# Kernel tuning notes

Measured on AMD Instinct MI355X. Metric: run time of the kernel, lower is better.

The kernel has to match this reference:

```python
import jax, jax.numpy as jnp
import numpy as np

Q_HEADS, KV_HEADS, HEAD_DIM, WINDOW = 16, 4, 128, 512
HIDDEN = 2048
ROPE_BASE = 10000.0


def _rope_tables(T, head_dim, dtype):
    half = head_dim // 2
    inv_freq = 1.0 / (ROPE_BASE ** (jnp.arange(half, dtype=jnp.float32) / half))
    t = jnp.arange(T, dtype=jnp.float32)
    freqs = jnp.outer(t, inv_freq)  # [T, half]
    return jnp.cos(freqs).astype(dtype), jnp.sin(freqs).astype(dtype)


def _apply_rope(x, cos, sin):
    # x: [B, T, H, D]; cos/sin: [T, D//2] -> broadcast [1, T, 1, D//2]
    c = cos[None, :, None, :]
    s = sin[None, :, None, :]
    x1, x2 = jnp.split(x, 2, axis=-1)
    return jnp.concatenate([x1 * c - x2 * s, x1 * s + x2 * c], axis=-1)


def setup_inputs() -> dict:
    key = jax.random.key(0)
    ks = jax.random.split(key, 5)
    B, T = 1, 4096
    x = jax.random.normal(ks[0], (B, T, HIDDEN), dtype=jnp.float32)
    sc = 0.02
    wq = jax.random.normal(ks[1], (Q_HEADS * HEAD_DIM, HIDDEN), dtype=jnp.float32) * sc
    wk = jax.random.normal(ks[2], (KV_HEADS * HEAD_DIM, HIDDEN), dtype=jnp.float32) * sc
    wv = jax.random.normal(ks[3], (KV_HEADS * HEAD_DIM, HIDDEN), dtype=jnp.float32) * sc
    wo = jax.random.normal(ks[4], (HIDDEN, Q_HEADS * HEAD_DIM), dtype=jnp.float32) * sc
    return {"x": x, "wq": wq, "wk": wk, "wv": wv, "wo": wo}


def reference(x, wq, wk, wv, wo):
    B, T, _ = x.shape
    reps = Q_HEADS // KV_HEADS
    scale = 1.0 / np.sqrt(HEAD_DIM)

    q = jnp.einsum('bth,oh->bto', x, wq).reshape(B, T, Q_HEADS, HEAD_DIM)
    k = jnp.einsum('bth,oh->bto', x, wk).reshape(B, T, KV_HEADS, HEAD_DIM)
    v = jnp.einsum('bth,oh->bto', x, wv).reshape(B, T, KV_HEADS, HEAD_DIM)

    cos, sin = _rope_tables(T, HEAD_DIM, x.dtype)
    q = _apply_rope(q, cos, sin)
    k = _apply_rope(k, cos, sin)

    # GQA without materializing repeated K/V: group q as [B,T,KVH,reps,D]
    qg = q.reshape(B, T, KV_HEADS, reps, HEAD_DIM)
    scores = jnp.einsum('btgrd,bsgd->bgrts', qg, k) * scale  # [B,KVH,reps,T,T]

    idx = jnp.arange(T)
    # allowed: causal (s <= t) AND within window (t - s <= WINDOW)
    allowed = (idx[None, :] <= idx[:, None]) & (idx[:, None] - idx[None, :] <= WINDOW)
    scores = jnp.where(allowed[None, None, None], scores, jnp.finfo(scores.dtype).min)
    probs = jax.nn.softmax(scores, axis=-1)

    out = jnp.einsum('bgrts,bsgd->btgrd', probs, v)  # [B,T,KVH,reps,D]
    out = out.reshape(B, T, Q_HEADS * HEAD_DIM)
    return jnp.einsum('bto,ho->bth', out, wo)
```

## Files before the change

### kernel.cpp

```cpp
#include <hip/hip_runtime.h>

typedef __attribute__((ext_vector_type(8))) short short8;
typedef __attribute__((ext_vector_type(4))) float f32x4;
typedef __attribute__((ext_vector_type(4))) unsigned short u16x4;

__device__ __forceinline__ unsigned short f2b(float f) {
  unsigned int u = __float_as_uint(f);
  u += 0x7fffu + ((u >> 16) & 1u);
  return (unsigned short)(u >> 16);
}
__device__ __forceinline__ void glds16(const void* g, void* l) {
  __builtin_amdgcn_global_load_lds(
      (const __attribute__((address_space(1))) unsigned int*)g,
      (__attribute__((address_space(3))) unsigned int*)l, 16, 0, 0);
}

__global__ __launch_bounds__(256) void cast_all(const float* __restrict__ x,
                                                const float* __restrict__ wq,
                                                const float* __restrict__ wk,
                                                const float* __restrict__ wv,
                                                const float* __restrict__ wo,
                                                unsigned short* __restrict__ dst) {
  const int i = blockIdx.x * 256 + threadIdx.x;
  const float* s;
  int off;
  if (i < 2097152)      { s = x;  off = i; }
  else if (i < 3145728) { s = wq; off = i - 2097152; }
  else if (i < 3407872) { s = wk; off = i - 3145728; }
  else if (i < 3670016) { s = wv; off = i - 3407872; }
  else                  { s = wo; off = i - 3670016; }
  f32x4 v = ((const f32x4*)s)[off];
  u16x4 o;
  o[0] = f2b(v[0]); o[1] = f2b(v[1]); o[2] = f2b(v[2]); o[3] = f2b(v[3]);
  ((u16x4*)dst)[i] = o;
}

__global__ __launch_bounds__(512, 2) void gemm256(
    const unsigned short* __restrict__ A, const unsigned short* __restrict__ B,
    const int Karg, const int mode,
    unsigned short* __restrict__ qb, unsigned short* __restrict__ kb,
    unsigned short* __restrict__ vtg, float* __restrict__ Cout, const int Narg) {
  extern __shared__ char smem[];
  const int tid = threadIdx.x;
  const int w = tid >> 6, lane = tid & 63;
  const int quad = lane >> 4, l15 = lane & 15;
  const int wm = w >> 2, wn = w & 3;
  const int m0 = blockIdx.x * 256, n0 = blockIdx.y * 256;

  int nb[4];
#pragma unroll
  for (int ni = 0; ni < 4; ++ni) {
    const int bbi = (wn & 1) * 4 + ni;
    nb[ni] = mode ? ((bbi & 1) ? 4 + (bbi >> 1) : (bbi >> 1)) : bbi;
  }

  const int fragOff = l15 * 64 + ((quad * 16) ^ ((l15 & 8) << 2));
  char* const aWave = smem + wm * 16384;
  char* const bWave = smem + 32768 + (wn >> 1) * 16384;

  const int sr = lane >> 2;
  const int sc = ((lane & 3) * 8) ^ ((lane & 32) ? 16 : 0);
  const unsigned short* const Abase = A + (size_t)(m0 + (w >> 1) * 16 + sr) * 2048 + (w & 1) * 32 + sc;
  const unsigned short* const Bbase = B + (size_t)(n0 + (w >> 1) * 16 + sr) * 2048 + (w & 1) * 32 + sc;

#define BARF()                            \
  asm volatile("" ::: "memory");          \
  __builtin_amdgcn_s_barrier();           \
  asm volatile("" ::: "memory");

#define STAGE_AJ(h, tt, jj)                                                              \
  {                                                                                      \
    const int t_ = ((tt) < 32) ? (tt) : 31;                                              \
    glds16(Abase + (size_t)(h) * (128 * 2048) + (jj) * (64 * 2048) + (size_t)t_ * 64,    \
           smem + (t_ & 1) * 65536 + (h) * 16384 + (jj) * 8192 + w * 1024);              \
  }
#define STAGE_B2(h, tt)                                                                  \
  {                                                                                      \
    const int t_ = ((tt) < 32) ? (tt) : 31;                                              \
    char* const d_ = smem + (t_ & 1) * 65536 + 32768 + (h) * 16384 + w * 1024;           \
    glds16(Bbase + (size_t)(h) * (128 * 2048) + (size_t)t_ * 64, d_);                    \
    glds16(Bbase + (size_t)(h) * (128 * 2048) + (64 * 2048) + (size_t)t_ * 64, d_ + 8192); \
  }
#define RD_A(dst, c, MI0)                                                                \
  _Pragma("unroll") for (int mi = 0; mi < 4; ++mi)                                       \
  _Pragma("unroll") for (int kk = 0; kk < 2; ++kk)                                       \
      dst[mi][kk] = *(const short8*)(aWave + (c) * 65536 + (((MI0) + mi) * 2 + kk) * 1024 + fragOff);
#define RD_B(dst, c, NI0)                                                                \
  _Pragma("unroll") for (int ni = 0; ni < 2; ++ni)                                       \
  _Pragma("unroll") for (int kk = 0; kk < 2; ++kk)                                       \
      dst[ni][kk] = *(const short8*)(bWave + (c) * 65536 + (nb[(NI0) + ni] * 2 + kk) * 1024 + fragOff);

  f32x4 acc[8][4];
  const f32x4 fz = {0.f, 0.f, 0.f, 0.f};
#pragma unroll
  for (int i = 0; i < 8; ++i)
#pragma unroll
    for (int j = 0; j < 4; ++j) acc[i][j] = fz;

  short8 af[4][2], blo[2][2], bhi[2][2];

#define MFMA_Q(MOFF, NOFF, BF)                                                   \
  _Pragma("unroll") for (int mi = 0; mi < 4; ++mi)                               \
  _Pragma("unroll") for (int ni = 0; ni < 2; ++ni)                               \
  _Pragma("unroll") for (int kk = 0; kk < 2; ++kk)                               \
      acc[(MOFF) + mi][(NOFF) + ni] = __builtin_amdgcn_mfma_f32_16x16x32_bf16(   \
          af[mi][kk], BF[ni][kk], acc[(MOFF) + mi][(NOFF) + ni], 0, 0, 0);

  STAGE_AJ(0, 0, 0) STAGE_AJ(1, 0, 0) STAGE_B2(0, 0) STAGE_B2(1, 0) STAGE_AJ(0, 0, 1) STAGE_AJ(1, 0, 1)
  STAGE_AJ(0, 1, 0) STAGE_AJ(1, 1, 0) STAGE_B2(0, 1) STAGE_B2(1, 1) STAGE_AJ(0, 1, 1) STAGE_AJ(1, 1, 1)
  asm volatile("s_waitcnt vmcnt(8)" ::: "memory");
  __builtin_amdgcn_s_barrier();
  asm volatile("" ::: "memory");
  RD_A(af, 0, 0)
  RD_B(blo, 0, 0)

#define HALF(c, tt)                                                                  \
                                                                             \
  BARF()                                                                             \
  __builtin_amdgcn_s_setprio(1); MFMA_Q(0, 0, blo) __builtin_amdgcn_s_setprio(0);    \
  RD_B(bhi, (c), 2)                                                                  \
  BARF()                                                                             \
   STAGE_AJ(0, (tt) + 2, 0) STAGE_AJ(1, (tt) + 2, 0)                         \
  BARF()                                                                             \
  __builtin_amdgcn_s_setprio(1); MFMA_Q(0, 2, bhi) __builtin_amdgcn_s_setprio(0);    \
  RD_A(af, (c), 4)                                                                   \
  BARF()                                                                             \
   STAGE_B2(0, (tt) + 2) STAGE_B2(1, (tt) + 2)                               \
  BARF()                                                                             \
  __builtin_amdgcn_s_setprio(1); MFMA_Q(4, 2, bhi) __builtin_amdgcn_s_setprio(0);    \
  BARF()                                                                             \
   STAGE_AJ(0, (tt) + 2, 1) STAGE_AJ(1, (tt) + 2, 1)                         \
  BARF()                                                                             \
  __builtin_amdgcn_s_setprio(1); MFMA_Q(4, 0, blo) __builtin_amdgcn_s_setprio(0);    \
  asm volatile("s_waitcnt vmcnt(8)" ::: "memory");                                   \
  RD_A(af, (c) ^ 1, 0)                                                               \
  RD_B(blo, (c) ^ 1, 0)

#pragma unroll 1
  for (int T = 0; T < 32; T += 2) {
    HALF(0, T)
    HALF(1, T + 1)
  }
  asm volatile("s_waitcnt vmcnt(0)" ::: "memory");
#undef HALF
#undef MFMA_Q
#undef RD_A
#undef RD_B
#undef STAGE_AJ
#undef STAGE_B2
#undef BARF

  if (mode == 0) {
    const int colBase = n0 + wn * 64;
#pragma unroll
    for (int mi = 0; mi < 8; ++mi) {
      const int row = m0 + wm * 128 + mi * 16 + quad * 4;
#pragma unroll
      for (int ni = 0; ni < 4; ++ni) {
        const int col = colBase + ni * 16 + l15;
#pragma unroll
        for (int r = 0; r < 4; ++r)
          Cout[(size_t)(row + r) * 2048 + col] = acc[mi][ni][r];
      }
    }
    return;
  }

  const int y = blockIdx.y;
  const int tb0 = m0 + wm * 128;
  if (y >= 10) {
    const int g = (y - 10) * 2 + (wn >> 1);
#pragma unroll
    for (int mi = 0; mi < 8; ++mi) {
      const int tb = tb0 + mi * 16 + quad * 4;
#pragma unroll
      for (int ni = 0; ni < 4; ++ni) {
        const int d = nb[ni] * 16 + l15;
        u16x4 o;
#pragma unroll
        for (int r = 0; r < 4; ++r) o[r] = f2b(acc[mi][ni][r]);
        *(u16x4*)(vtg + (size_t)(g * 128 + d) * 4096 + tb) = o;
      }
    }
  } else {
    unsigned short* dst;
    int stride, hoff;
    if (y < 8) { dst = qb; stride = 2048; hoff = (y * 2 + (wn >> 1)) * 128; }
    else       { dst = kb; stride = 512;  hoff = ((y - 8) * 2 + (wn >> 1)) * 128; }
    const float c2 = 0.20762050593045889f;
    const float inv2pi = 0.15915494309189535f;
#pragma unroll
    for (int j = 0; j < 2; ++j) {
      const int i = ((wn & 1) * 2 + j) * 16 + l15;
      const float inv_rev = exp2f(-(float)i * c2) * inv2pi;
#pragma unroll
      for (int mi = 0; mi < 8; ++mi) {
#pragma unroll
        for (int r = 0; r < 4; ++r) {
          const int t = tb0 + mi * 16 + quad * 4 + r;
          float rev = (float)t * inv_rev;
          rev -= floorf(rev);
          const float sn = __builtin_amdgcn_sinf(rev);
          const float cs = __builtin_amdgcn_cosf(rev);
          const float x1 = acc[mi][2 * j][r], x2 = acc[mi][2 * j + 1][r];
          unsigned short* p = dst + (size_t)t * stride + hoff + i;
          p[0]  = f2b(x1 * cs - x2 * sn);
          p[64] = f2b(x1 * sn + x2 * cs);
        }
      }
    }
  }
}

__global__ __launch_bounds__(512) void attn_fwd(const unsigned short* __restrict__ qp,
                                                const unsigned short* __restrict__ kp,
                                                const unsigned short* __restrict__ vtg,
                                                unsigned short* __restrict__ op) {
  __shared__ unsigned short Ks[2][4][1024];
  __shared__ unsigned short Vt[2][4096];
  const int tid = threadIdx.x;
  const int w = tid >> 6, lane = tid & 63;
  const int quad = lane >> 4, l15 = lane & 15;
  const int t0 = blockIdx.x * 64;
  const int g = blockIdx.y;
  const int h = g * 4 + (w & 3);
  const int t0w = t0 + (w >> 2) * 32;
  const f32x4 fzero = {0.f, 0.f, 0.f, 0.f};
  const float scale = 0.088388347648318447f;
  const float NEG_INF = -__builtin_inff();

  short8 qf[4][2];
#pragma unroll
  for (int qt = 0; qt < 2; qt++) {
    const unsigned short* qrow = qp + (size_t)(t0w + qt * 16 + l15) * 2048 + h * 128 + quad * 8;
#pragma unroll
    for (int kb = 0; kb < 4; kb++) qf[kb][qt] = *(const short8*)(qrow + kb * 32);
  }

  f32x4 oacc[8][2];
#pragma unroll
  for (int db = 0; db < 8; db++) { oacc[db][0] = fzero; oacc[db][1] = fzero; }
  float Mrow[2] = {-1.0e30f, -1.0e30f}, Lrow[2] = {0.f, 0.f};

  const int s_begin = (t0 >= 512) ? (t0 - 512) : 0;
  const int nch = ((t0 + 63 - s_begin) >> 5) + 1;

  const int r4 = lane >> 2, c4 = lane & 3;
#define ATTN_STAGE(s0_, b_)                                                              \
  {                                                                                      \
    const int s0v = (s0_);                                                               \
    if (w < 4) {                                                                         \
      _Pragma("unroll")                                                                  \
      for (int p = 0; p < 2; p++)                                                        \
        glds16(kp + (size_t)(s0v + p * 16 + r4) * 512 + g * 128 + w * 32 + c4 * 8,       \
               &Ks[b_][w][p * 512]);                                                     \
    } else {                                                                             \
      const int wv = w - 4;                                                              \
      _Pragma("unroll")                                                                  \
      for (int p = 0; p < 2; p++)                                                        \
        glds16(vtg + (size_t)(g * 128 + wv * 32 + p * 16 + r4) * 4096 + s0v + c4 * 8,    \
               &Vt[b_][wv * 1024 + p * 512]);                                            \
    }                                                                                    \
  }

  ATTN_STAGE(s_begin, 0);

  for (int c = 0; c < nch; ++c) {
    const int s0 = s_begin + c * 32;
    const int b = c & 1;
    __syncthreads();
    if (c + 1 < nch) ATTN_STAGE(s_begin + (c + 1) * 32, (c + 1) & 1);

    if (s0 + 31 >= t0w - 512 && s0 <= t0w + 31) {
      f32x4 sacc[2][2];
      sacc[0][0] = fzero; sacc[0][1] = fzero; sacc[1][0] = fzero; sacc[1][1] = fzero;
      const int permBase = ((l15 >> 2) << 3) + (l15 & 3);
#pragma unroll
      for (int kb = 0; kb < 4; kb++) {
        short8 af0 = *(const short8*)&Ks[b][kb][(permBase + 0) * 32 + quad * 8];
        short8 af1 = *(const short8*)&Ks[b][kb][(permBase + 4) * 32 + quad * 8];
        sacc[0][0] = __builtin_amdgcn_mfma_f32_16x16x32_bf16(af0, qf[kb][0], sacc[0][0], 0, 0, 0);
        sacc[0][1] = __builtin_amdgcn_mfma_f32_16x16x32_bf16(af0, qf[kb][1], sacc[0][1], 0, 0, 0);
        sacc[1][0] = __builtin_amdgcn_mfma_f32_16x16x32_bf16(af1, qf[kb][0], sacc[1][0], 0, 0, 0);
        sacc[1][1] = __builtin_amdgcn_mfma_f32_16x16x32_bf16(af1, qf[kb][1], sacc[1][1], 0, 0, 0);
      }

      short8 pb[2];
      float alpha[2];
#pragma unroll
      for (int qt = 0; qt < 2; qt++) {
        const int tq = t0w + qt * 16 + l15;
        float vals[8];
        float cmax = NEG_INF;
#pragma unroll
        for (int kt = 0; kt < 2; kt++)
#pragma unroll
          for (int r = 0; r < 4; r++) {
            const int s = s0 + quad * 8 + kt * 4 + r;
            const bool ok = (unsigned)(tq - s) <= 512u;
            const float v = ok ? sacc[kt][qt][r] * scale : NEG_INF;
            vals[kt * 4 + r] = v;
            cmax = fmaxf(cmax, v);
          }
        cmax = fmaxf(cmax, __shfl_xor(cmax, 16));
        cmax = fmaxf(cmax, __shfl_xor(cmax, 32));
        const float Mnew = fmaxf(Mrow[qt], cmax);
        alpha[qt] = __expf(Mrow[qt] - Mnew);
        Mrow[qt] = Mnew;
        float csum = 0.f;
#pragma unroll
        for (int j = 0; j < 8; j++) {
          const float p = __expf(vals[j] - Mnew);
          csum += p;
          pb[qt][j] = (short)f2b(p);
        }
        csum += __shfl_xor(csum, 16);
        csum += __shfl_xor(csum, 32);
        Lrow[qt] = Lrow[qt] * alpha[qt] + csum;
      }

#pragma unroll
      for (int db = 0; db < 8; db++) {
        short8 vf = *(const short8*)&Vt[b][(db * 16 + l15) * 32 + quad * 8];
#pragma unroll
        for (int qt = 0; qt < 2; qt++) {
          oacc[db][qt][0] *= alpha[qt]; oacc[db][qt][1] *= alpha[qt];
          oacc[db][qt][2] *= alpha[qt]; oacc[db][qt][3] *= alpha[qt];
          oacc[db][qt] = __builtin_amdgcn_mfma_f32_16x16x32_bf16(vf, pb[qt], oacc[db][qt], 0, 0, 0);
        }
      }
    }
  }
#undef ATTN_STAGE

#pragma unroll
  for (int qt = 0; qt < 2; qt++) {
    const float invL = 1.f / Lrow[qt];
    unsigned short* orow = op + (size_t)(t0w + qt * 16 + l15) * 2048 + h * 128;
#pragma unroll
    for (int db = 0; db < 8; db++) {
      u16x4 o;
#pragma unroll
      for (int r = 0; r < 4; r++) o[r] = f2b(oacc[db][qt][r] * invL);
      *(u16x4*)(orow + db * 16 + quad * 4) = o;
    }
  }
}

extern "C" void kernel_launch(void* const* d_in, const int* in_sizes, int n_in,
                              void* d_out, int out_size, void* d_ws, size_t ws_size,
                              hipStream_t stream) {
  const float* x  = (const float*)d_in[0];
  const float* wq = (const float*)d_in[1];
  const float* wk = (const float*)d_in[2];
  const float* wv = (const float*)d_in[3];
  const float* wo = (const float*)d_in[4];
  float* out = (float*)d_out;
  char* ws = (char*)d_ws;

  unsigned short* xb    = (unsigned short*)(ws + 0);
  unsigned short* wqkv  = (unsigned short*)(ws + 16777216);
  unsigned short* wob   = (unsigned short*)(ws + 29360128);
  unsigned short* qb    = (unsigned short*)(ws + 37748736);
  unsigned short* kbuf  = (unsigned short*)(ws + 54525952);
  unsigned short* vtg   = (unsigned short*)(ws + 58720256);
  unsigned short* attnb = xb;

  static bool attr_done = false;
  if (!attr_done) {
    hipFuncSetAttribute(reinterpret_cast<const void*>(gemm256),
                        hipFuncAttributeMaxDynamicSharedMemorySize, 131072);
    attr_done = true;
  }

  cast_all<<<18432, 256, 0, stream>>>(x, wq, wk, wv, wo, (unsigned short*)ws);

  gemm256<<<dim3(16, 12), 512, 131072, stream>>>(xb, wqkv, 2048, 1,
                                                 qb, kbuf, vtg, nullptr, 0);

  attn_fwd<<<dim3(64, 4), 512, 0, stream>>>(qb, kbuf, vtg, attnb);

  gemm256<<<dim3(16, 8), 512, 131072, stream>>>(attnb, wob, 2048, 0,
                                                nullptr, nullptr, nullptr, out, 2048);
}
```

Measured before the change: 261.8 us.

## Add 128x256-tile output-projection GEMM kernel for more blocks

```diff
diff --git a/kernel.cpp b/kernel.cpp
--- a/kernel.cpp
+++ b/kernel.cpp
@@ -212,6 +212,118 @@
   }
 }
 
+__global__ __launch_bounds__(512, 2) void gemm128(const unsigned short* __restrict__ A,
+                                                  const unsigned short* __restrict__ B,
+                                                  float* __restrict__ Cout) {
+  extern __shared__ char smem[];
+  const int tid = threadIdx.x;
+  const int w = tid >> 6, lane = tid & 63;
+  const int quad = lane >> 4, l15 = lane & 15;
+  const int wm = w >> 2, wn = w & 3;
+  const int m0 = blockIdx.x * 128, n0 = blockIdx.y * 256;
+
+  const int fragOff = l15 * 64 + ((quad * 16) ^ ((l15 & 8) << 2));
+  char* const aWave = smem;
+  char* const bWave = smem + 16384 + (wn >> 1) * 16384;
+
+  const int sr = lane >> 2;
+  const int sc = ((lane & 3) * 8) ^ ((lane & 32) ? 16 : 0);
+  const unsigned short* const Abase = A + (size_t)(m0 + (w >> 1) * 16 + sr) * 2048 + (w & 1) * 32 + sc;
+  const unsigned short* const Bbase = B + (size_t)(n0 + (w >> 1) * 16 + sr) * 2048 + (w & 1) * 32 + sc;
+
+#define BARF()                            \
+  asm volatile("" ::: "memory");          \
+  __builtin_amdgcn_s_barrier();           \
+  asm volatile("" ::: "memory");
+
+#define G_STAGE_A(tt)                                                                    \
+  {                                                                                      \
+    const int t_ = ((tt) < 32) ? (tt) : 31;                                              \
+    char* const d_ = smem + (t_ & 1) * 49152 + w * 1024;                                 \
+    glds16(Abase + (size_t)t_ * 64, d_);                                                 \
+    glds16(Abase + (64 * 2048) + (size_t)t_ * 64, d_ + 8192);                            \
+  }
+#define G_STAGE_B(h, tt)                                                                 \
+  {                                                                                      \
+    const int t_ = ((tt) < 32) ? (tt) : 31;                                              \
+    char* const d_ = smem + (t_ & 1) * 49152 + 16384 + (h) * 16384 + w * 1024;           \
+    glds16(Bbase + (size_t)(h) * (128 * 2048) + (size_t)t_ * 64, d_);                    \
+    glds16(Bbase + (size_t)(h) * (128 * 2048) + (64 * 2048) + (size_t)t_ * 64, d_ + 8192); \
+  }
+#define G_RD_A(c)                                                                        \
+  _Pragma("unroll") for (int mi = 0; mi < 4; ++mi)                                       \
+  _Pragma("unroll") for (int kk = 0; kk < 2; ++kk)                                       \
+      af[mi][kk] = *(const short8*)(aWave + (c) * 49152 + ((wm * 4 + mi) * 2 + kk) * 1024 + fragOff);
+#define G_RD_B(dst, c, NI0)                                                              \
+  _Pragma("unroll") for (int ni = 0; ni < 2; ++ni)                                       \
+  _Pragma("unroll") for (int kk = 0; kk < 2; ++kk)                                       \
+      dst[ni][kk] = *(const short8*)(bWave + (c) * 49152 + (((wn & 1) * 4 + (NI0) + ni) * 2 + kk) * 1024 + fragOff);
+
+  f32x4 acc[4][4];
+  const f32x4 fz = {0.f, 0.f, 0.f, 0.f};
+#pragma unroll
+  for (int i = 0; i < 4; ++i)
+#pragma unroll
+    for (int j = 0; j < 4; ++j) acc[i][j] = fz;
+
+  short8 af[4][2], blo[2][2], bhi[2][2];
+
+#define G_MFMA(NOFF, BF)                                                         \
+  _Pragma("unroll") for (int mi = 0; mi < 4; ++mi)                               \
+  _Pragma("unroll") for (int ni = 0; ni < 2; ++ni)                               \
+  _Pragma("unroll") for (int kk = 0; kk < 2; ++kk)                               \
+      acc[mi][(NOFF) + ni] = __builtin_amdgcn_mfma_f32_16x16x32_bf16(            \
+          af[mi][kk], BF[ni][kk], acc[mi][(NOFF) + ni], 0, 0, 0);
+
+  G_STAGE_A(0) G_STAGE_B(0, 0) G_STAGE_B(1, 0) G_STAGE_A(1)
+  asm volatile("s_waitcnt vmcnt(2)" ::: "memory");
+  __builtin_amdgcn_s_barrier();
+  asm volatile("" ::: "memory");
+  G_RD_A(0)
+  G_RD_B(blo, 0, 0)
+
+#define G_TILE(c, tt)                                                                \
+   G_STAGE_B(0, (tt) + 1) G_STAGE_B(1, (tt) + 1)                             \
+  BARF()                                                                             \
+  __builtin_amdgcn_s_setprio(1); G_MFMA(0, blo) __builtin_amdgcn_s_setprio(0);       \
+  G_RD_B(bhi, (c), 2)                                                                \
+  BARF()                                                                             \
+   G_STAGE_A((tt) + 2)                                                       \
+  BARF()                                                                             \
+  __builtin_amdgcn_s_setprio(1); G_MFMA(2, bhi) __builtin_amdgcn_s_setprio(0);       \
+  asm volatile("s_waitcnt vmcnt(2)" ::: "memory");                                   \
+  G_RD_A((c) ^ 1)                                                                    \
+  G_RD_B(blo, (c) ^ 1, 0)                                                            \
+  BARF()
+
+#pragma unroll 1
+  for (int T = 0; T < 32; T += 2) {
+    G_TILE(0, T)
+    G_TILE(1, T + 1)
+  }
+  asm volatile("s_waitcnt vmcnt(0)" ::: "memory");
+#undef G_TILE
+#undef G_MFMA
+#undef G_RD_A
+#undef G_RD_B
+#undef G_STAGE_A
+#undef G_STAGE_B
+#undef BARF
+
+  const int colBase = n0 + wn * 64;
+#pragma unroll
+  for (int mi = 0; mi < 4; ++mi) {
+    const int row = m0 + wm * 64 + mi * 16 + quad * 4;
+#pragma unroll
+    for (int ni = 0; ni < 4; ++ni) {
+      const int col = colBase + ni * 16 + l15;
+#pragma unroll
+      for (int r = 0; r < 4; ++r)
+        Cout[(size_t)(row + r) * 2048 + col] = acc[mi][ni][r];
+    }
+  }
+}
+
 __global__ __launch_bounds__(512) void attn_fwd(const unsigned short* __restrict__ qp,
                                                 const unsigned short* __restrict__ kp,
                                                 const unsigned short* __restrict__ vtg,
@@ -370,6 +482,8 @@
   if (!attr_done) {
     hipFuncSetAttribute(reinterpret_cast<const void*>(gemm256),
                         hipFuncAttributeMaxDynamicSharedMemorySize, 131072);
+    hipFuncSetAttribute(reinterpret_cast<const void*>(gemm128),
+                        hipFuncAttributeMaxDynamicSharedMemorySize, 98304);
     attr_done = true;
   }
 
@@ -380,6 +494,5 @@
 
   attn_fwd<<<dim3(64, 4), 512, 0, stream>>>(qb, kbuf, vtg, attnb);
 
-  gemm256<<<dim3(16, 8), 512, 131072, stream>>>(attnb, wob, 2048, 0,
-                                                nullptr, nullptr, nullptr, out, 2048);
-}
+  gemm128<<<dim3(32, 8), 512, 98304, stream>>>(attnb, wob, out);
+}
```

Result: faster. 248.6 us (-5.0%).
